# Kernel optimization log

Measured on AMD Instinct MI355X. Metric: run time of the kernel, lower is better.

Reference implementation:

```python
import jax, jax.numpy as jnp
import numpy as np
import math

D_MODEL = 1024
H = 16
D_K = D_MODEL // H
B = 4
S = 2048
NEG = -1e9


def setup_inputs() -> dict:
    key = jax.random.key(0)
    ks = jax.random.split(key, 11)
    scale = 1.0 / math.sqrt(D_MODEL)
    inp = {
        'q': jax.random.normal(ks[0], (B, S, D_MODEL), dtype=jnp.float32),
        'k': jax.random.normal(ks[1], (B, S, D_MODEL), dtype=jnp.float32),
        'v': jax.random.normal(ks[2], (B, S, D_MODEL), dtype=jnp.float32),
        'wq': jax.random.normal(ks[3], (D_MODEL, D_MODEL), dtype=jnp.float32) * scale,
        'bq': jnp.zeros((D_MODEL,), dtype=jnp.float32),
        'wk': jax.random.normal(ks[4], (D_MODEL, D_MODEL), dtype=jnp.float32) * scale,
        'bk': jnp.zeros((D_MODEL,), dtype=jnp.float32),
        'wv': jax.random.normal(ks[5], (D_MODEL, D_MODEL), dtype=jnp.float32) * scale,
        'bv': jnp.zeros((D_MODEL,), dtype=jnp.float32),
        'wo': jax.random.normal(ks[6], (D_MODEL, D_MODEL), dtype=jnp.float32) * scale,
        'bo': jnp.zeros((D_MODEL,), dtype=jnp.float32),
        # broadcastable causal mask [1, 1, S, S]; 0 = masked out
        'mask': jnp.tril(jnp.ones((S, S), dtype=jnp.int32))[None, None, :, :],
    }
    return inp


def reference(q, k, v, wq, bq, wk, bk, wv, bv, wo, bo, mask):
    # QKV projections: x @ W^T + b (nn.Linear convention)
    def split_heads(x):  # [B, S, D] -> [B, H, S, d_k]
        return x.reshape(B, S, H, D_K).transpose(0, 2, 1, 3)

    query = split_heads(q @ wq.T + bq)
    key_ = split_heads(k @ wk.T + bk)
    value = split_heads(v @ wv.T + bv)

    # scaled dot-product attention with mask; scores: [B, H, S, S]
    scores = jnp.einsum('bhqd,bhkd->bhqk', query, key_) / math.sqrt(D_K)
    scores = jnp.where(mask == 0, jnp.float32(NEG), scores)
    attn = jax.nn.softmax(scores, axis=-1)
    ctx = jnp.einsum('bhqk,bhkd->bhqd', attn, value)  # [B, H, S, d_k]

    # merge heads and output projection
    ctx = ctx.transpose(0, 2, 1, 3).reshape(B, S, D_MODEL)
    return ctx @ wo.T + bo
```

## Files before the change

kernel.cpp:

```cpp
#include <hip/hip_runtime.h>

#define DEVI __device__ __forceinline__

typedef __attribute__((ext_vector_type(8))) __bf16 bf16x8;
typedef __attribute__((ext_vector_type(4))) float f32x4;
typedef __attribute__((ext_vector_type(16))) float f32x16;
typedef __attribute__((ext_vector_type(4))) unsigned uint32x4;

DEVI __bf16 f2bf(float f) {
  unsigned u = __builtin_bit_cast(unsigned, f);
  unsigned r = u + 0x7fffu + ((u >> 16) & 1u);
  unsigned short h = (unsigned short)(r >> 16);
  return __builtin_bit_cast(__bf16, h);
}

DEVI unsigned cvt_pk_bf16(float lo, float hi) {
  unsigned r;
  asm("v_cvt_pk_bf16_f32 %0, %1, %2" : "=v"(r) : "v"(lo), "v"(hi));
  return r;
}

DEVI void load_lds16(const void* g, void* l) {
  __builtin_amdgcn_global_load_lds((__attribute__((address_space(1))) const void*)g,
                                   (__attribute__((address_space(3))) void*)l,
                                   16, 0, 0);
}

__global__ void convert_w4(const float* __restrict__ w0, const float* __restrict__ w1,
                           const float* __restrict__ w2, const float* __restrict__ w3,
                           __bf16* __restrict__ o0, __bf16* __restrict__ o1,
                           __bf16* __restrict__ o2, __bf16* __restrict__ o3, int n8) {
  int stride = gridDim.x * blockDim.x;
  for (int i = blockIdx.x * blockDim.x + threadIdx.x; i < 4 * n8; i += stride) {
    int sel = i / n8, j = i - sel * n8;
    const float* in = sel == 0 ? w0 : sel == 1 ? w1 : sel == 2 ? w2 : w3;
    __bf16* out = sel == 0 ? o0 : sel == 1 ? o1 : sel == 2 ? o2 : o3;
    float4 a = ((const float4*)in)[j * 2];
    float4 b = ((const float4*)in)[j * 2 + 1];
    bf16x8 o;
    o[0] = f2bf(a.x); o[1] = f2bf(a.y); o[2] = f2bf(a.z); o[3] = f2bf(a.w);
    o[4] = f2bf(b.x); o[5] = f2bf(b.y); o[6] = f2bf(b.z); o[7] = f2bf(b.w);
    ((bf16x8*)out)[j] = o;
  }
}

__global__ __launch_bounds__(256, 3) void gemm_qkv(
    const float* __restrict__ qa, const float* __restrict__ ka, const float* __restrict__ va,
    const __bf16* __restrict__ Wq, const __bf16* __restrict__ Wk, const __bf16* __restrict__ Wv,
    const float* __restrict__ bq, const float* __restrict__ bk, const float* __restrict__ bv,
    __bf16* __restrict__ Qh, __bf16* __restrict__ Kh, __bf16* __restrict__ Vt)
{
  __shared__ __align__(16) __bf16 As[2][128 * 32];
  __shared__ __align__(16) __bf16 Bs[2][128 * 32];
  const int sel = blockIdx.z;
  const float* A = sel == 0 ? qa : sel == 1 ? ka : va;
  const __bf16* W = sel == 0 ? Wq : sel == 1 ? Wk : Wv;
  const float* bias = sel == 0 ? bq : sel == 1 ? bk : bv;
  __bf16* outp = sel == 0 ? Qh : sel == 1 ? Kh : Vt;
  const bool vmode = (sel == 2);

  const int tid = threadIdx.x;
  const int lane = tid & 63;
  const int ln = lane & 15, g = lane >> 4;
  const int w = tid >> 6;
  const int wr = w >> 1, wc = w & 1;
  const int id = blockIdx.y * 64 + blockIdx.x;
  const int bx = 8 * (id & 7) + ((id >> 3) & 7);
  const int by = id >> 6;
  const int row0 = bx * 128, col0 = by * 128;

  const int ar = tid >> 1, ah = tid & 1;
  const int axr = (ar >> 1) & 3;

  f32x4 acc[4][4] = {};
  float4 fA[4];

  auto issueA = [&](int kt) {
    const float4* src = (const float4*)&A[(size_t)(row0 + ar) * 1024 + kt * 32 + ah * 16];
#pragma unroll
    for (int j = 0; j < 4; ++j) fA[j] = src[j];
  };
  auto issueW = [&](int buf, int kt) {
#pragma unroll
    for (int i = 0; i < 2; ++i) {
      int c = tid + 256 * i;
      int r = c >> 2, sl = c & 3;
      int so = 8 * (sl ^ ((r >> 1) & 3));
      load_lds16(&W[(size_t)(col0 + r) * 1024 + kt * 32 + so], &Bs[buf][c * 8]);
    }
  };
  auto writeA = [&](int buf) {
#pragma unroll
    for (int j = 0; j < 2; ++j) {
      uint32x4 o;
      o[0] = cvt_pk_bf16(fA[2 * j].x, fA[2 * j].y);
      o[1] = cvt_pk_bf16(fA[2 * j].z, fA[2 * j].w);
      o[2] = cvt_pk_bf16(fA[2 * j + 1].x, fA[2 * j + 1].y);
      o[3] = cvt_pk_bf16(fA[2 * j + 1].z, fA[2 * j + 1].w);
      int s = 2 * ah + j;
      *(uint32x4*)&As[buf][ar * 32 + (s ^ axr) * 8] = o;
    }
  };
  auto compute = [&](int buf) {
    const __bf16* as = As[buf];
    const __bf16* bs = Bs[buf];
    bf16x8 aF[4], bF[4];
#pragma unroll
    for (int mi = 0; mi < 4; ++mi) {
      int r = wr * 64 + mi * 16 + ln;
      aF[mi] = *(const bf16x8*)&as[r * 32 + ((g * 8) ^ (((r >> 1) & 3) * 8))];
    }
#pragma unroll
    for (int ni = 0; ni < 4; ++ni) {
      int r = wc * 64 + ni * 16 + ln;
      bF[ni] = *(const bf16x8*)&bs[r * 32 + ((g * 8) ^ (((r >> 1) & 3) * 8))];
    }
    __builtin_amdgcn_s_setprio(1);
#pragma unroll
    for (int mi = 0; mi < 4; ++mi)
#pragma unroll
      for (int ni = 0; ni < 4; ++ni)
        acc[mi][ni] = __builtin_amdgcn_mfma_f32_16x16x32_bf16(aF[mi], bF[ni], acc[mi][ni], 0, 0, 0);
    __builtin_amdgcn_s_setprio(0);
  };

  issueA(0); issueW(0, 0);
  writeA(0);
  __syncthreads();
#pragma unroll 1
  for (int kt = 0; kt < 32; ++kt) {
    const int cur = kt & 1, nxt = cur ^ 1;
    if (kt + 1 < 32) { issueA(kt + 1); issueW(nxt, kt + 1); }
    compute(cur);
    if (kt + 1 < 32) writeA(nxt);
    __syncthreads();
  }

#pragma unroll
  for (int ni = 0; ni < 4; ++ni) {
    int n = col0 + wc * 64 + ni * 16 + ln;
    float bv = bias[n];
#pragma unroll
    for (int mi = 0; mi < 4; ++mi) {
#pragma unroll
      for (int i = 0; i < 4; ++i) {
        int m = row0 + wr * 64 + mi * 16 + g * 4 + i;
        float val = acc[mi][ni][i] + bv;
        int b = m >> 11, s = m & 2047, h = n >> 6, d = n & 63;
        size_t idx = vmode
          ? ((size_t)((b * 16 + h) * 64 + d) * 2048 + s)
          : ((size_t)((b * 16 + h) * 2048 + s) * 64 + d);
        outp[idx] = f2bf(val);
      }
    }
  }
}

template<int MODE>
__global__ __launch_bounds__(256, 2) void gemm_bt(
    const __bf16* __restrict__ A, const __bf16* __restrict__ W,
    const float* __restrict__ bias, void* __restrict__ outp)
{
  __shared__ __bf16 As[3][128 * 32];
  __shared__ __bf16 Bs[3][128 * 32];
  const int tid = threadIdx.x;
  const int lane = tid & 63;
  const int ln = lane & 15, g = lane >> 4;
  const int w = tid >> 6;
  const int wr = w >> 1, wc = w & 1;
  const int id = blockIdx.y * 64 + blockIdx.x;
  const int bx = 8 * (id & 7) + ((id >> 3) & 7);
  const int by = id >> 6;
  const int row0 = bx * 128, col0 = by * 128;

  f32x4 acc[4][4] = {};

  auto stage = [&](int buf, int kt) {
    const int k0 = kt * 32;
#pragma unroll
    for (int i = 0; i < 2; ++i) {
      int c = tid + 256 * i;
      int r = c >> 2, sl = c & 3;
      int so = 8 * (sl ^ ((r >> 1) & 3));
      load_lds16(&A[(size_t)(row0 + r) * 1024 + k0 + so], &As[buf][c * 8]);
      load_lds16(&W[(size_t)(col0 + r) * 1024 + k0 + so], &Bs[buf][c * 8]);
    }
  };

  auto compute = [&](int buf) {
    const __bf16* as = As[buf];
    const __bf16* bs = Bs[buf];
    bf16x8 aF[4], bF[4];
#pragma unroll
    for (int mi = 0; mi < 4; ++mi) {
      int r = wr * 64 + mi * 16 + ln;
      aF[mi] = *(const bf16x8*)&as[r * 32 + ((g * 8) ^ (((r >> 1) & 3) * 8))];
    }
#pragma unroll
    for (int ni = 0; ni < 4; ++ni) {
      int r = wc * 64 + ni * 16 + ln;
      bF[ni] = *(const bf16x8*)&bs[r * 32 + ((g * 8) ^ (((r >> 1) & 3) * 8))];
    }
    __builtin_amdgcn_s_setprio(1);
#pragma unroll
    for (int mi = 0; mi < 4; ++mi)
#pragma unroll
      for (int ni = 0; ni < 4; ++ni)
        acc[mi][ni] = __builtin_amdgcn_mfma_f32_16x16x32_bf16(aF[mi], bF[ni], acc[mi][ni], 0, 0, 0);
    __builtin_amdgcn_s_setprio(0);
  };

  stage(0, 0);
  stage(1, 1);
#pragma unroll 1
  for (int kt = 0; kt < 31; ++kt) {
    asm volatile("s_waitcnt vmcnt(4)" ::: "memory");
    __builtin_amdgcn_s_barrier();
    asm volatile("" ::: "memory");
    if (kt + 2 < 32) stage((kt + 2) % 3, kt + 2);
    compute(kt % 3);
  }
  asm volatile("s_waitcnt vmcnt(0)" ::: "memory");
  __builtin_amdgcn_s_barrier();
  asm volatile("" ::: "memory");
  compute(31 % 3);

#pragma unroll
  for (int ni = 0; ni < 4; ++ni) {
    int n = col0 + wc * 64 + ni * 16 + ln;
    float bv = bias[n];
#pragma unroll
    for (int mi = 0; mi < 4; ++mi) {
#pragma unroll
      for (int i = 0; i < 4; ++i) {
        int m = row0 + wr * 64 + mi * 16 + g * 4 + i;
        float val = acc[mi][ni][i] + bv;
        if (MODE == 2) {
          ((float*)outp)[(size_t)m * 1024 + n] = val;
        } else {
          int b = m >> 11, s = m & 2047, h = n >> 6, d = n & 63;
          size_t idx = (MODE == 0)
            ? ((size_t)((b * 16 + h) * 2048 + s) * 64 + d)
            : ((size_t)((b * 16 + h) * 64 + d) * 2048 + s);
          ((__bf16*)outp)[idx] = f2bf(val);
        }
      }
    }
  }
}

__global__ __launch_bounds__(512, 4) void attn_fwd(
    const __bf16* __restrict__ Qh, const __bf16* __restrict__ Kh,
    const __bf16* __restrict__ Vt, __bf16* __restrict__ Ctx)
{
  __shared__ __bf16 KVs[8][64 * 64];

  const int tid = threadIdx.x;
  const int lane = tid & 63;
  const int l31 = lane & 31, hl = lane >> 5;
  const int w = tid >> 6;
  const int wq3 = w & 3, p = w >> 2;
  const int bh = blockIdx.x;
  const int b = bh >> 4, h = bh & 15;
  const float CE = 0.18033688f;
  const float MC = 40.0f * CE;

  auto stagePair = [&](int tp) {
    const int base = 2 * (tp & 1);
    const int c = tid;
    const int r = c >> 3, sl = c & 7;
    const int so = 8 * (sl ^ (r & 7));
#pragma unroll
    for (int i = 0; i < 2; ++i) {
      const int kv0 = (2 * tp + i) * 64, s = base + i;
      load_lds16(&Kh[((size_t)bh * 2048 + kv0 + r) * 64 + so], &KVs[s][c * 8]);
      load_lds16(&Vt[((size_t)bh * 64 + r) * 2048 + kv0 + so], &KVs[4 + s][c * 8]);
    }
  };

  auto strip = [&](int qb) {
    const int q0 = qb * 128;
    const int qw = q0 + wq3 * 32;
    const int qglob = qw + l31;
    const int np = qb + 1;

    bf16x8 qF[4];
#pragma unroll
    for (int ds = 0; ds < 4; ++ds)
      qF[ds] = *(const bf16x8*)&Qh[((size_t)bh * 2048 + qglob) * 64 + ds * 16 + hl * 8];

    f32x16 oT[2] = {};
    float lrun = 0.f;

    __syncthreads();
    stagePair(0);
    for (int tp = 0; tp < np; ++tp) {
      __syncthreads();
      if (tp + 1 < np) stagePair(tp + 1);
      const int kv0 = (2 * tp + p) * 64;
      if (kv0 > qw + 31) continue;
      const __bf16* ksm = KVs[2 * (tp & 1) + p];
      const __bf16* vsm = KVs[4 + 2 * (tp & 1) + p];

      f32x16 sT[2] = {};
#pragma unroll
      for (int kblk = 0; kblk < 2; ++kblk) {
        bf16x8 aK[4];
        const int r = kblk * 32 + l31;
#pragma unroll
        for (int ds = 0; ds < 4; ++ds)
          aK[ds] = *(const bf16x8*)&ksm[r * 64 + ((ds * 16 + hl * 8) ^ ((r & 7) * 8))];
        __builtin_amdgcn_s_setprio(1);
#pragma unroll
        for (int ds = 0; ds < 4; ++ds)
          sT[kblk] = __builtin_amdgcn_mfma_f32_32x32x16_bf16(aK[ds], qF[ds], sT[kblk], 0, 0, 0);
        __builtin_amdgcn_s_setprio(0);
      }

      if (kv0 + 63 > qw) {
#pragma unroll
        for (int kblk = 0; kblk < 2; ++kblk)
#pragma unroll
          for (int r = 0; r < 16; ++r) {
            int kvg = kv0 + kblk * 32 + (r & 3) + 8 * (r >> 2) + 4 * hl;
            sT[kblk][r] = (kvg <= qglob) ? sT[kblk][r] : -3e38f;
          }
      }

      unsigned c0[8], c1[8];
      float ps0 = 0.f, ps1 = 0.f, ps2 = 0.f, ps3 = 0.f;
#pragma unroll
      for (int w2 = 0; w2 < 8; ++w2) {
        float p0 = exp2f(__builtin_fmaf(sT[0][2 * w2],     CE, -MC));
        float p1 = exp2f(__builtin_fmaf(sT[0][2 * w2 + 1], CE, -MC));
        float p2 = exp2f(__builtin_fmaf(sT[1][2 * w2],     CE, -MC));
        float p3 = exp2f(__builtin_fmaf(sT[1][2 * w2 + 1], CE, -MC));
        ps0 += p0; ps1 += p1; ps2 += p2; ps3 += p3;
        c0[w2] = cvt_pk_bf16(p0, p1);
        c1[w2] = cvt_pk_bf16(p2, p3);
      }
      lrun += (ps0 + ps1) + (ps2 + ps3);

      uint32x4 Wv[4];
#pragma unroll
      for (int kblk = 0; kblk < 2; ++kblk)
#pragma unroll
        for (int ksl = 0; ksl < 2; ++ksl)
#pragma unroll
          for (int al = 0; al < 2; ++al) {
            unsigned cp = kblk ? c1[4 * ksl + al]     : c0[4 * ksl + al];
            unsigned cq = kblk ? c1[4 * ksl + 2 + al] : c0[4 * ksl + 2 + al];
            unsigned cqx = __shfl_xor(cq, 32);
            unsigned cpx = __shfl_xor(cp, 32);
            Wv[kblk * 2 + ksl][al]     = hl ? cqx : cp;
            Wv[kblk * 2 + ksl][al + 2] = hl ? cq  : cpx;
          }

#pragma unroll
      for (int dblk = 0; dblk < 2; ++dblk) {
        bf16x8 aV[4];
        const int r = dblk * 32 + l31;
#pragma unroll
        for (int ks = 0; ks < 4; ++ks)
          aV[ks] = *(const bf16x8*)&vsm[r * 64 + ((ks * 16 + hl * 8) ^ ((r & 7) * 8))];
        __builtin_amdgcn_s_setprio(1);
#pragma unroll
        for (int ks = 0; ks < 4; ++ks)
          oT[dblk] = __builtin_amdgcn_mfma_f32_32x32x16_bf16(
              aV[ks], __builtin_bit_cast(bf16x8, Wv[ks]), oT[dblk], 0, 0, 0);
        __builtin_amdgcn_s_setprio(0);
      }
    }

    __syncthreads();
    float* ex = (float*)KVs + wq3 * 2176 + lane * 34;
    if (p == 1) {
      lrun += __shfl_xor(lrun, 32);
#pragma unroll
      for (int dblk = 0; dblk < 2; ++dblk)
#pragma unroll
        for (int rb = 0; rb < 8; ++rb)
          *(float2*)(ex + dblk * 16 + rb * 2) =
              make_float2(oT[dblk][2 * rb], oT[dblk][2 * rb + 1]);
      ex[32] = lrun;
    }
    __syncthreads();
    if (p == 0) {
      lrun += __shfl_xor(lrun, 32);
      lrun += ex[32];
#pragma unroll
      for (int dblk = 0; dblk < 2; ++dblk)
#pragma unroll
        for (int rb = 0; rb < 8; ++rb) {
          float2 v = *(float2*)(ex + dblk * 16 + rb * 2);
          oT[dblk][2 * rb]     += v.x;
          oT[dblk][2 * rb + 1] += v.y;
        }
      const float inv = 1.0f / fmaxf(lrun, 1e-30f);
#pragma unroll
      for (int dblk = 0; dblk < 2; ++dblk)
#pragma unroll
        for (int rb = 0; rb < 4; ++rb) {
          unsigned u0 = cvt_pk_bf16(oT[dblk][4 * rb]     * inv, oT[dblk][4 * rb + 1] * inv);
          unsigned u1 = cvt_pk_bf16(oT[dblk][4 * rb + 2] * inv, oT[dblk][4 * rb + 3] * inv);
          int d = dblk * 32 + rb * 8 + 4 * hl;
          size_t idx = ((size_t)(b * 2048 + qglob)) * 1024 + h * 64 + d;
          *(uint2*)&Ctx[idx] = make_uint2(u0, u1);
        }
    }
  };

  strip(15 - (int)blockIdx.y);
  strip((int)blockIdx.y);
}

extern "C" void kernel_launch(void* const* d_in, const int* in_sizes, int n_in,
                              void* d_out, int out_size, void* d_ws, size_t ws_size,
                              hipStream_t stream) {
  const float* q  = (const float*)d_in[0];
  const float* k  = (const float*)d_in[1];
  const float* v  = (const float*)d_in[2];
  const float* wq = (const float*)d_in[3];
  const float* bq = (const float*)d_in[4];
  const float* wk = (const float*)d_in[5];
  const float* bk = (const float*)d_in[6];
  const float* wv = (const float*)d_in[7];
  const float* bv = (const float*)d_in[8];
  const float* wo = (const float*)d_in[9];
  const float* bo = (const float*)d_in[10];
  float* out = (float*)d_out;
  char* ws = (char*)d_ws;

  const size_t MB = 1024 * 1024;
  __bf16* Wqb  = (__bf16*)(ws + 0 * MB);
  __bf16* Wkb  = (__bf16*)(ws + 2 * MB);
  __bf16* Wvb  = (__bf16*)(ws + 4 * MB);
  __bf16* Wob  = (__bf16*)(ws + 6 * MB);
  __bf16* Ctx  = (__bf16*)(ws + 8 * MB);
  __bf16* Qh   = (__bf16*)(ws + 24 * MB);
  __bf16* Kh   = (__bf16*)(ws + 40 * MB);
  __bf16* Vt   = (__bf16*)(ws + 56 * MB);

  const int W8 = 1024 * 1024 / 8;

  convert_w4<<<2048, 256, 0, stream>>>(wq, wk, wv, wo, Wqb, Wkb, Wvb, Wob, W8);

  gemm_qkv<<<dim3(64, 8, 3), 256, 0, stream>>>(q, k, v, Wqb, Wkb, Wvb,
                                               bq, bk, bv, Qh, Kh, Vt);

  attn_fwd<<<dim3(64, 8), 512, 0, stream>>>(Qh, Kh, Vt, Ctx);

  gemm_bt<2><<<dim3(64, 8), 256, 0, stream>>>(Ctx, Wob, bo, out);
}
```

Before: 204.5 us.

## Deepen QKV GEMM pipeline to triple-buffered LDS with two-ahead prefetch

Moves the QKV projection GEMM from double-buffered to triple-buffered LDS and issues global loads two k-tiles ahead, using two fp32 register staging sets. Barriers become manual s_waitcnt vmcnt plus s_barrier, so a wait no longer drains all outstanding loads. The main loop is unrolled by six to keep buffer indices static, with an explicit epilogue for the last tiles. This hides more global-load latency, at the cost of more LDS per block (possible occupancy loss at 3 blocks/CU) and more registers, and it depends on exact vmcnt counting being correct.

Measured after the change: 206.4 us. Within noise of the previous version (+0.9%).

```diff
diff --git a/kernel.cpp b/kernel.cpp
--- a/kernel.cpp
+++ b/kernel.cpp
@@ -50,8 +50,8 @@
     const float* __restrict__ bq, const float* __restrict__ bk, const float* __restrict__ bv,
     __bf16* __restrict__ Qh, __bf16* __restrict__ Kh, __bf16* __restrict__ Vt)
 {
-  __shared__ __align__(16) __bf16 As[2][128 * 32];
-  __shared__ __align__(16) __bf16 Bs[2][128 * 32];
+  __shared__ __align__(16) __bf16 As[3][128 * 32];
+  __shared__ __align__(16) __bf16 Bs[3][128 * 32];
   const int sel = blockIdx.z;
   const float* A = sel == 0 ? qa : sel == 1 ? ka : va;
   const __bf16* W = sel == 0 ? Wq : sel == 1 ? Wk : Wv;
@@ -73,12 +73,12 @@
   const int axr = (ar >> 1) & 3;
 
   f32x4 acc[4][4] = {};
-  float4 fA[4];
-
-  auto issueA = [&](int kt) {
+  float4 fa0[4], fa1[4];
+
+  auto issueA = [&](int kt, float4* f) {
     const float4* src = (const float4*)&A[(size_t)(row0 + ar) * 1024 + kt * 32 + ah * 16];
 #pragma unroll
-    for (int j = 0; j < 4; ++j) fA[j] = src[j];
+    for (int j = 0; j < 4; ++j) f[j] = src[j];
   };
   auto issueW = [&](int buf, int kt) {
 #pragma unroll
@@ -89,14 +89,14 @@
       load_lds16(&W[(size_t)(col0 + r) * 1024 + kt * 32 + so], &Bs[buf][c * 8]);
     }
   };
-  auto writeA = [&](int buf) {
+  auto writeA = [&](int buf, const float4* f) {
 #pragma unroll
     for (int j = 0; j < 2; ++j) {
       uint32x4 o;
-      o[0] = cvt_pk_bf16(fA[2 * j].x, fA[2 * j].y);
-      o[1] = cvt_pk_bf16(fA[2 * j].z, fA[2 * j].w);
-      o[2] = cvt_pk_bf16(fA[2 * j + 1].x, fA[2 * j + 1].y);
-      o[3] = cvt_pk_bf16(fA[2 * j + 1].z, fA[2 * j + 1].w);
+      o[0] = cvt_pk_bf16(f[2 * j].x, f[2 * j].y);
+      o[1] = cvt_pk_bf16(f[2 * j].z, f[2 * j].w);
+      o[2] = cvt_pk_bf16(f[2 * j + 1].x, f[2 * j + 1].y);
+      o[3] = cvt_pk_bf16(f[2 * j + 1].z, f[2 * j + 1].w);
       int s = 2 * ah + j;
       *(uint32x4*)&As[buf][ar * 32 + (s ^ axr) * 8] = o;
     }
@@ -124,17 +124,40 @@
     __builtin_amdgcn_s_setprio(0);
   };
 
-  issueA(0); issueW(0, 0);
-  writeA(0);
-  __syncthreads();
+#define QKV_BAR(N) \
+  asm volatile("s_waitcnt vmcnt(" #N ") lgkmcnt(0)" ::: "memory"); \
+  __builtin_amdgcn_s_barrier(); \
+  asm volatile("" ::: "memory");
+
+#define QKV_STEP(KT, E, FAC, FAN) \
+  QKV_BAR(6) \
+  issueA((KT) + 2, FAC); \
+  issueW(((E) + 2) % 3, (KT) + 2); \
+  compute((E) % 3); \
+  writeA(((E) + 1) % 3, FAN);
+
+  issueA(0, fa0); issueW(0, 0);
+  issueA(1, fa1); issueW(1, 1);
+  writeA(0, fa0);
+
 #pragma unroll 1
-  for (int kt = 0; kt < 32; ++kt) {
-    const int cur = kt & 1, nxt = cur ^ 1;
-    if (kt + 1 < 32) { issueA(kt + 1); issueW(nxt, kt + 1); }
-    compute(cur);
-    if (kt + 1 < 32) writeA(nxt);
-    __syncthreads();
+  for (int u = 0; u < 5; ++u) {
+    const int kt = 6 * u;
+    QKV_STEP(kt + 0, 0, fa0, fa1)
+    QKV_STEP(kt + 1, 1, fa1, fa0)
+    QKV_STEP(kt + 2, 2, fa0, fa1)
+    QKV_STEP(kt + 3, 3, fa1, fa0)
+    QKV_STEP(kt + 4, 4, fa0, fa1)
+    QKV_STEP(kt + 5, 5, fa1, fa0)
   }
+  QKV_BAR(6)
+  compute(0);
+  asm volatile("s_waitcnt vmcnt(2)" ::: "memory");
+  writeA(1, fa1);
+  QKV_BAR(0)
+  compute(1);
+#undef QKV_STEP
+#undef QKV_BAR
 
 #pragma unroll
   for (int ni = 0; ni < 4; ++ni) {
```
